# Kernel tuning notes

Measured on AMD Instinct MI355X. Metric: run time of the kernel, lower is better.

The kernel has to match this reference:

```python
import jax, jax.numpy as jnp
import numpy as np

ALPHA_LEAKY = 0.2
EPS = 1e-10


def setup_inputs() -> dict:
    key = jax.random.key(0)
    k1, k2, k3, k4 = jax.random.split(key, 4)
    N, E, IN_DIM, OUT_DIM = 50000, 800000, 128, 64
    node_features = jax.random.normal(k1, (N, IN_DIM), dtype=jnp.float32)
    edge_index = jax.random.randint(k2, (2, E), 0, N, dtype=jnp.int64)
    # xavier_uniform with gain=1.414
    def xavier(k, shape, gain=1.414):
        fan_in, fan_out = shape[1], shape[0]
        bound = gain * np.sqrt(6.0 / (fan_in + fan_out))
        return jax.random.uniform(k, shape, jnp.float32, -bound, bound)
    W = xavier(k3, (OUT_DIM, IN_DIM))          # nn.Linear weight layout [out, in]
    a = xavier(k4, (1, 2 * OUT_DIM))           # attention vector [1, 2*out]
    return {"node_features": node_features, "edge_index": edge_index, "W": W, "a": a}


def reference(node_features, edge_index, W, a):
    # h = W(node_features): [N, out_dim]
    h = node_features @ W.T
    num_nodes, out_dim = h.shape
    src = edge_index[0]
    tgt = edge_index[1]
    # a @ cat([h_src, h_tgt]) decomposes into per-node partial scores (no [E, 2d] concat)
    s_src = h @ a[0, :out_dim]   # [N]
    s_tgt = h @ a[0, out_dim:]   # [N]
    e = jax.nn.leaky_relu(s_src[src] + s_tgt[tgt], negative_slope=ALPHA_LEAKY)  # [E]
    # segment softmax over incoming edges of each target node
    e_max = jax.ops.segment_max(e, tgt, num_segments=num_nodes)
    e_exp = jnp.exp(e - e_max[tgt])
    e_sum = jax.ops.segment_sum(e_exp, tgt, num_segments=num_nodes)
    attention = e_exp / (e_sum[tgt] + EPS)
    # weighted scatter-add aggregation of source features into targets
    h_prime = jax.ops.segment_sum(h[src] * attention[:, None], tgt, num_segments=num_nodes)
    return jax.nn.elu(h_prime)
```

## Files before the change

### kernel.cpp

```cpp
#include <hip/hip_runtime.h>
#include <math.h>

#define ALPHA_LEAKY 0.2f
#define EPS_F 1e-10f
#define NBMAX 1024

typedef __attribute__((ext_vector_type(8))) short short8;
typedef __attribute__((ext_vector_type(4))) float f32x4;

__device__ __forceinline__ unsigned short bf16_rne(float f) {
    unsigned u = __float_as_uint(f);
    u += 0x7FFFu + ((u >> 16) & 1u);
    return (unsigned short)(u >> 16);
}

__global__ void k_prep(const float* __restrict__ W, uint4* __restrict__ Wbf) {
    int f = blockIdx.x * 256 + threadIdx.x;
    int nt = f >> 8;
    if (nt >= 4) return;
    int l = f & 63, kt = (f >> 6) & 3;
    int nn = nt * 16 + (l & 15);
    int k  = kt * 32 + (l >> 4) * 8;
    const float* wr = W + nn * 128 + k;
    unsigned short b[8];
    #pragma unroll
    for (int j = 0; j < 8; ++j) b[j] = bf16_rne(wr[j]);
    uint4 v;
    v.x = (unsigned)b[0] | ((unsigned)b[1] << 16);
    v.y = (unsigned)b[2] | ((unsigned)b[3] << 16);
    v.z = (unsigned)b[4] | ((unsigned)b[5] << 16);
    v.w = (unsigned)b[6] | ((unsigned)b[7] << 16);
    Wbf[f] = v;
}

__global__ __launch_bounds__(256) void k_gemm(
    const float* __restrict__ X, const uint4* __restrict__ Wbf,
    const float* __restrict__ a, unsigned short* __restrict__ hb,
    float* __restrict__ s_src, float* __restrict__ s_tgt, int n, int nstripes) {
    const int lane = threadIdx.x & 63;
    const int ml = lane & 15, g = lane >> 4;
    short8 bfr[4][4];
    #pragma unroll
    for (int nt = 0; nt < 4; ++nt)
        #pragma unroll
        for (int kt = 0; kt < 4; ++kt) {
            uint4 v = Wbf[(nt * 4 + kt) * 64 + lane];
            bfr[nt][kt] = *(short8*)&v;
        }
    float as[4], at[4];
    #pragma unroll
    for (int nt = 0; nt < 4; ++nt) {
        as[nt] = a[nt * 16 + ml];
        at[nt] = a[64 + nt * 16 + ml];
    }
    for (int stripe = blockIdx.x * 4 + (threadIdx.x >> 6); stripe < nstripes;
         stripe += gridDim.x * 4) {
        const int row0 = stripe * 16;
        const int rrow = min(row0 + ml, n - 1);
        const float* xr = X + (size_t)rrow * 128;
        f32x4 acc[4] = {{0.f,0.f,0.f,0.f},{0.f,0.f,0.f,0.f},
                        {0.f,0.f,0.f,0.f},{0.f,0.f,0.f,0.f}};
        #pragma unroll
        for (int kt = 0; kt < 4; ++kt) {
            float4 x0 = *(const float4*)(xr + kt * 32 + g * 8);
            float4 x1 = *(const float4*)(xr + kt * 32 + g * 8 + 4);
            short8 af;
            af[0] = (short)bf16_rne(x0.x); af[1] = (short)bf16_rne(x0.y);
            af[2] = (short)bf16_rne(x0.z); af[3] = (short)bf16_rne(x0.w);
            af[4] = (short)bf16_rne(x1.x); af[5] = (short)bf16_rne(x1.y);
            af[6] = (short)bf16_rne(x1.z); af[7] = (short)bf16_rne(x1.w);
            #pragma unroll
            for (int nt = 0; nt < 4; ++nt)
                acc[nt] = __builtin_amdgcn_mfma_f32_16x16x32_bf16(
                    af, bfr[nt][kt], acc[nt], 0, 0, 0);
        }
        #pragma unroll
        for (int reg = 0; reg < 4; ++reg) {
            int row = row0 + g * 4 + reg;
            float p = acc[0][reg] * as[0] + acc[1][reg] * as[1] +
                      acc[2][reg] * as[2] + acc[3][reg] * as[3];
            float q = acc[0][reg] * at[0] + acc[1][reg] * at[1] +
                      acc[2][reg] * at[2] + acc[3][reg] * at[3];
            #pragma unroll
            for (int off = 1; off < 16; off <<= 1) {
                p += __shfl_xor(p, off, 64);
                q += __shfl_xor(q, off, 64);
            }
            if (ml == 0 && row < n) { s_src[row] = p; s_tgt[row] = q; }
        }
        #pragma unroll
        for (int nt = 0; nt < 4; ++nt)
            #pragma unroll
            for (int reg = 0; reg < 4; ++reg) {
                int row = row0 + g * 4 + reg;
                if (row < n)
                    hb[(size_t)row * 64 + nt * 16 + ml] = bf16_rne(acc[nt][reg]);
            }
    }
}

__global__ __launch_bounds__(256) void k_hist(
    const int* __restrict__ ei, int* __restrict__ histg, int nb, int E, int epb) {
    __shared__ int hist[NBMAX];
    const int t = threadIdx.x;
    for (int k = t; k < nb; k += 256) hist[k] = 0;
    __syncthreads();
    const int e0 = blockIdx.x * epb, e1 = min(e0 + epb, E);
    for (int e = e0 + t; e < e1; e += 256)
        atomicAdd(&hist[ei[E + e] >> 6], 1);
    __syncthreads();
    int* outp = histg + (size_t)blockIdx.x * nb;
    for (int k = t; k < nb; k += 256) outp[k] = hist[k];
}

__global__ __launch_bounds__(256) void k_colscan(
    int* __restrict__ histg, int* __restrict__ btot, int nb) {
    __shared__ int wsum[4];
    const int bucket = blockIdx.x;
    const int t = threadIdx.x, lane = t & 63, w = t >> 6;
    int v = histg[(size_t)t * nb + bucket];
    int pre = v;
    #pragma unroll
    for (int off = 1; off < 64; off <<= 1) {
        int x = __shfl_up(pre, off, 64);
        if (lane >= off) pre += x;
    }
    if (lane == 63) wsum[w] = pre;
    __syncthreads();
    int wb = 0;
    for (int k = 0; k < w; ++k) wb += wsum[k];
    histg[(size_t)t * nb + bucket] = wb + pre - v;
    if (t == 255) btot[bucket] = wb + pre;
}

__global__ __launch_bounds__(256) void k_bscan(
    const int* __restrict__ btot, int* __restrict__ bstart, int nb, int E) {
    __shared__ int wsum[4];
    int t = threadIdx.x;
    int lane = t & 63, w = t >> 6;
    int v[4]; int sum = 0;
    #pragma unroll
    for (int j = 0; j < 4; ++j) {
        int idx = t * 4 + j;
        v[j] = (idx < nb) ? btot[idx] : 0;
        sum += v[j];
    }
    int pre = sum;
    #pragma unroll
    for (int off = 1; off < 64; off <<= 1) {
        int x = __shfl_up(pre, off, 64);
        if (lane >= off) pre += x;
    }
    if (lane == 63) wsum[w] = pre;
    __syncthreads();
    int wbase = 0;
    for (int k = 0; k < w; ++k) wbase += wsum[k];
    int run = wbase + pre - sum;
    #pragma unroll
    for (int j = 0; j < 4; ++j) {
        int idx = t * 4 + j;
        if (idx < nb) bstart[idx] = run;
        run += v[j];
    }
    if (t == 255) bstart[nb] = E;
}

__global__ __launch_bounds__(256) void k_place(
    const int* __restrict__ ei, const int* __restrict__ histg,
    const int* __restrict__ bstart, int2* __restrict__ st,
    int nb, int E, int epb) {
    __shared__ int cur[NBMAX];
    const int t = threadIdx.x;
    const int* my = histg + (size_t)blockIdx.x * nb;
    for (int k = t; k < nb; k += 256) cur[k] = bstart[k] + my[k];
    __syncthreads();
    const int e0 = blockIdx.x * epb, e1 = min(e0 + epb, E);
    for (int e = e0 + t; e < e1; e += 256) {
        int s  = ei[e];
        int tt = ei[E + e];
        int slot = atomicAdd(&cur[tt >> 6], 1);
        st[slot] = make_int2(s, tt);
    }
}

__global__ __launch_bounds__(256) void k_local(
    const int2* __restrict__ st, const int* __restrict__ bstart,
    int* __restrict__ base, int* __restrict__ deg, int* __restrict__ csr_src,
    int n) {
    __shared__ int hist[64];
    __shared__ int nbase[64];
    const int b = blockIdx.x;
    const int n0 = b << 6;
    const int t = threadIdx.x;
    if (t < 64) hist[t] = 0;
    __syncthreads();
    const int s0 = bstart[b], s1 = bstart[b + 1];
    for (int i = s0 + t; i < s1; i += 256)
        atomicAdd(&hist[st[i].y - n0], 1);
    __syncthreads();
    if (t < 64) {
        int v = hist[t];
        int pre = v;
        #pragma unroll
        for (int off = 1; off < 64; off <<= 1) {
            int x = __shfl_up(pre, off, 64);
            if (t >= off) pre += x;
        }
        int bs = s0 + pre - v;
        nbase[t] = bs;
        if (n0 + t < n) { base[n0 + t] = bs; deg[n0 + t] = v; }
    }
    __syncthreads();
    if (t < 64) hist[t] = nbase[t];
    __syncthreads();
    for (int i = s0 + t; i < s1; i += 256) {
        int2 e = st[i];
        int slot = atomicAdd(&hist[e.y - n0], 1);
        csr_src[slot] = e.x;
    }
}

__device__ __forceinline__ void accum8(float acc[8], uint4 hv, float w) {
    unsigned u[4] = {hv.x, hv.y, hv.z, hv.w};
    #pragma unroll
    for (int i = 0; i < 4; ++i) {
        float lo = __uint_as_float(u[i] << 16);
        float hi = __uint_as_float(u[i] & 0xFFFF0000u);
        acc[2 * i]     = fmaf(w, lo, acc[2 * i]);
        acc[2 * i + 1] = fmaf(w, hi, acc[2 * i + 1]);
    }
}

__global__ __launch_bounds__(256) void k_node(
    const int* __restrict__ base, const int* __restrict__ deg,
    const int* __restrict__ csr_src, const float* __restrict__ s_src,
    const float* __restrict__ s_tgt, const unsigned short* __restrict__ hb,
    float* __restrict__ out, int n) {
    const int lane = threadIdx.x & 63;
    const int node = blockIdx.x * 4 + (threadIdx.x >> 6);
    if (node >= n) return;
    const int b = base[node];
    const int d = deg[node];
    const float st = s_tgt[node];
    const int g = lane >> 3, r = lane & 7;
    float acc[8] = {0.f, 0.f, 0.f, 0.f, 0.f, 0.f, 0.f, 0.f};

    if (d <= 64) {
        int src_l = 0; float w_l = 0.f, v = -INFINITY;
        if (lane < d) {
            src_l = csr_src[b + lane];
            float x = s_src[src_l] + st;
            v = (x > 0.f) ? x : ALPHA_LEAKY * x;
        }
        float m = v;
        #pragma unroll
        for (int off = 32; off > 0; off >>= 1) m = fmaxf(m, __shfl_xor(m, off, 64));
        float ex = (lane < d) ? expf(v - m) : 0.f;
        float sum = ex;
        #pragma unroll
        for (int off = 32; off > 0; off >>= 1) sum += __shfl_xor(sum, off, 64);
        w_l = ex * (1.f / (sum + EPS_F));
        for (int k = 0; k < d; k += 8) {
            int ke = k + g;
            int s   = __shfl(src_l, ke, 64);
            float w = __shfl(w_l,  ke, 64);
            uint4 hv = ((const uint4*)(hb + (size_t)s * 64))[r];
            accum8(acc, hv, w);
        }
    } else {
        float m = -INFINITY;
        for (int c = lane; c < d; c += 64) {
            float x = s_src[csr_src[b + c]] + st;
            x = (x > 0.f) ? x : ALPHA_LEAKY * x;
            m = fmaxf(m, x);
        }
        #pragma unroll
        for (int off = 32; off > 0; off >>= 1) m = fmaxf(m, __shfl_xor(m, off, 64));
        float sum = 0.f;
        for (int c = lane; c < d; c += 64) {
            float x = s_src[csr_src[b + c]] + st;
            x = (x > 0.f) ? x : ALPHA_LEAKY * x;
            sum += expf(x - m);
        }
        #pragma unroll
        for (int off = 32; off > 0; off >>= 1) sum += __shfl_xor(sum, off, 64);
        float inv = 1.f / (sum + EPS_F);
        for (int c0 = 0; c0 < d; c0 += 64) {
            int j = c0 + lane;
            int src_l = 0; float w_l = 0.f;
            if (j < d) {
                src_l = csr_src[b + j];
                float x = s_src[src_l] + st;
                x = (x > 0.f) ? x : ALPHA_LEAKY * x;
                w_l = expf(x - m) * inv;
            }
            int lim = min(64, d - c0);
            for (int k = 0; k < lim; k += 8) {
                int ke = k + g;
                int s   = __shfl(src_l, ke, 64);
                float w = __shfl(w_l,  ke, 64);
                uint4 hv = ((const uint4*)(hb + (size_t)s * 64))[r];
                accum8(acc, hv, w);
            }
        }
    }

    #pragma unroll
    for (int off = 8; off <= 32; off <<= 1) {
        #pragma unroll
        for (int j = 0; j < 8; ++j) acc[j] += __shfl_xor(acc[j], off, 64);
    }
    if (g == 0) {
        float4 o0, o1;
        o0.x = acc[0] > 0.f ? acc[0] : expf(acc[0]) - 1.f;
        o0.y = acc[1] > 0.f ? acc[1] : expf(acc[1]) - 1.f;
        o0.z = acc[2] > 0.f ? acc[2] : expf(acc[2]) - 1.f;
        o0.w = acc[3] > 0.f ? acc[3] : expf(acc[3]) - 1.f;
        o1.x = acc[4] > 0.f ? acc[4] : expf(acc[4]) - 1.f;
        o1.y = acc[5] > 0.f ? acc[5] : expf(acc[5]) - 1.f;
        o1.z = acc[6] > 0.f ? acc[6] : expf(acc[6]) - 1.f;
        o1.w = acc[7] > 0.f ? acc[7] : expf(acc[7]) - 1.f;
        float4* o4 = (float4*)out + (size_t)node * 16;
        o4[r * 2]     = o0;
        o4[r * 2 + 1] = o1;
    }
}

extern "C" void kernel_launch(void* const* d_in, const int* in_sizes, int n_in,
                              void* d_out, int out_size, void* d_ws, size_t ws_size,
                              hipStream_t stream) {
    const float* X  = (const float*)d_in[0];
    const int*   ei = (const int*)d_in[1];
    const float* W  = (const float*)d_in[2];
    const float* a  = (const float*)d_in[3];
    float* out = (float*)d_out;

    const int N = in_sizes[0] / 128;
    const int E = in_sizes[1] / 2;
    const int nb = (N + 63) >> 6;
    const int NBLK = 256;
    const int epb = (E + NBLK - 1) / NBLK;

    char* p = (char*)d_ws;
    unsigned short* hb = (unsigned short*)p; p += (size_t)N * 64 * sizeof(unsigned short);
    uint4* Wbf    = (uint4*)p;  p += 1024 * sizeof(uint4);
    float* s_src  = (float*)p;  p += (size_t)N * sizeof(float);
    float* s_tgt  = (float*)p;  p += (size_t)N * sizeof(float);
    int*   deg    = (int*)p;    p += (size_t)N * sizeof(int);
    int*   base   = (int*)p;    p += (size_t)N * sizeof(int);
    int*   histg  = (int*)p;    p += (size_t)NBLK * nb * sizeof(int);
    int*   btot   = (int*)p;    p += (size_t)nb * sizeof(int);
    int*   bstart = (int*)p;    p += (size_t)(nb + 1) * sizeof(int);
    int*   csr_src= (int*)p;    p += (size_t)E * sizeof(int);
    int2*  st     = (int2*)p;

    const int nstripes = (N + 15) / 16;
    k_prep   <<<4, 256, 0, stream>>>(W, Wbf);
    k_gemm   <<<(nstripes + 3) / 4, 256, 0, stream>>>(X, Wbf, a, hb, s_src, s_tgt, N, nstripes);
    k_hist   <<<NBLK, 256, 0, stream>>>(ei, histg, nb, E, epb);
    k_colscan<<<nb, 256, 0, stream>>>(histg, btot, nb);
    k_bscan  <<<1, 256, 0, stream>>>(btot, bstart, nb, E);
    k_place  <<<NBLK, 256, 0, stream>>>(ei, histg, bstart, st, nb, E, epb);
    k_local  <<<nb, 256, 0, stream>>>(st, bstart, base, deg, csr_src, N);
    k_node   <<<(N + 3) / 4, 256, 0, stream>>>(base, deg, csr_src, s_src, s_tgt, hb, out, N);
}
```

Measured before the change: 146.7 us.

## Fuse local CSR build and node aggregation into bucket-level shared-memory kernel

```diff
diff --git a/kernel.cpp b/kernel.cpp
--- a/kernel.cpp
+++ b/kernel.cpp
@@ -4,6 +4,7 @@
 #define ALPHA_LEAKY 0.2f
 #define EPS_F 1e-10f
 #define NBMAX 1024
+#define NBLK 128
 
 typedef __attribute__((ext_vector_type(8))) short short8;
 typedef __attribute__((ext_vector_type(4))) float f32x4;
@@ -118,7 +119,7 @@
     __shared__ int wsum[4];
     const int bucket = blockIdx.x;
     const int t = threadIdx.x, lane = t & 63, w = t >> 6;
-    int v = histg[(size_t)t * nb + bucket];
+    int v = (t < NBLK) ? histg[(size_t)t * nb + bucket] : 0;
     int pre = v;
     #pragma unroll
     for (int off = 1; off < 64; off <<= 1) {
@@ -129,8 +130,8 @@
     __syncthreads();
     int wb = 0;
     for (int k = 0; k < w; ++k) wb += wsum[k];
-    histg[(size_t)t * nb + bucket] = wb + pre - v;
-    if (t == 255) btot[bucket] = wb + pre;
+    if (t < NBLK) histg[(size_t)t * nb + bucket] = wb + pre - v;
+    if (t == 255) btot[bucket] = wsum[0] + wsum[1] + wsum[2] + wsum[3];
 }
 
 __global__ __launch_bounds__(256) void k_bscan(
@@ -167,7 +168,7 @@
 
 __global__ __launch_bounds__(256) void k_place(
     const int* __restrict__ ei, const int* __restrict__ histg,
-    const int* __restrict__ bstart, int2* __restrict__ st,
+    const int* __restrict__ bstart, unsigned* __restrict__ st,
     int nb, int E, int epb) {
     __shared__ int cur[NBMAX];
     const int t = threadIdx.x;
@@ -179,150 +180,67 @@
         int s  = ei[e];
         int tt = ei[E + e];
         int slot = atomicAdd(&cur[tt >> 6], 1);
-        st[slot] = make_int2(s, tt);
-    }
-}
-
-__global__ __launch_bounds__(256) void k_local(
-    const int2* __restrict__ st, const int* __restrict__ bstart,
-    int* __restrict__ base, int* __restrict__ deg, int* __restrict__ csr_src,
-    int n) {
-    __shared__ int hist[64];
-    __shared__ int nbase[64];
+        st[slot] = ((unsigned)s << 6) | (unsigned)(tt & 63);
+    }
+}
+
+__global__ __launch_bounds__(256) void k_bnode(
+    const unsigned* __restrict__ st, const int* __restrict__ bstart,
+    const float* __restrict__ s_src, const float* __restrict__ s_tgt,
+    const unsigned short* __restrict__ hb, float* __restrict__ out, int n) {
+    __shared__ unsigned mkey[64];
+    __shared__ float msh[64];
+    __shared__ float ssum[64];
+    __shared__ float acc[64 * 64];
     const int b = blockIdx.x;
     const int n0 = b << 6;
     const int t = threadIdx.x;
-    if (t < 64) hist[t] = 0;
-    __syncthreads();
+    const int lane = t & 63;
+    const int w = t >> 6;
+
+    if (t < 64) { mkey[t] = 0u; ssum[t] = 0.f; }
+    for (int i = t; i < 4096; i += 256) acc[i] = 0.f;
+    __syncthreads();
+
     const int s0 = bstart[b], s1 = bstart[b + 1];
-    for (int i = s0 + t; i < s1; i += 256)
-        atomicAdd(&hist[st[i].y - n0], 1);
+
+    for (int i = s0 + t; i < s1; i += 256) {
+        unsigned p = st[i];
+        int s = p >> 6, dt = p & 63;
+        float x = s_src[s] + s_tgt[n0 + dt];
+        x = (x > 0.f) ? x : ALPHA_LEAKY * x;
+        unsigned u = __float_as_uint(x);
+        unsigned key = (u & 0x80000000u) ? ~u : (u | 0x80000000u);
+        atomicMax(&mkey[dt], key);
+    }
     __syncthreads();
     if (t < 64) {
-        int v = hist[t];
-        int pre = v;
-        #pragma unroll
-        for (int off = 1; off < 64; off <<= 1) {
-            int x = __shfl_up(pre, off, 64);
-            if (t >= off) pre += x;
-        }
-        int bs = s0 + pre - v;
-        nbase[t] = bs;
-        if (n0 + t < n) { base[n0 + t] = bs; deg[n0 + t] = v; }
-    }
-    __syncthreads();
-    if (t < 64) hist[t] = nbase[t];
-    __syncthreads();
-    for (int i = s0 + t; i < s1; i += 256) {
-        int2 e = st[i];
-        int slot = atomicAdd(&hist[e.y - n0], 1);
-        csr_src[slot] = e.x;
-    }
-}
-
-__device__ __forceinline__ void accum8(float acc[8], uint4 hv, float w) {
-    unsigned u[4] = {hv.x, hv.y, hv.z, hv.w};
-    #pragma unroll
-    for (int i = 0; i < 4; ++i) {
-        float lo = __uint_as_float(u[i] << 16);
-        float hi = __uint_as_float(u[i] & 0xFFFF0000u);
-        acc[2 * i]     = fmaf(w, lo, acc[2 * i]);
-        acc[2 * i + 1] = fmaf(w, hi, acc[2 * i + 1]);
-    }
-}
-
-__global__ __launch_bounds__(256) void k_node(
-    const int* __restrict__ base, const int* __restrict__ deg,
-    const int* __restrict__ csr_src, const float* __restrict__ s_src,
-    const float* __restrict__ s_tgt, const unsigned short* __restrict__ hb,
-    float* __restrict__ out, int n) {
-    const int lane = threadIdx.x & 63;
-    const int node = blockIdx.x * 4 + (threadIdx.x >> 6);
-    if (node >= n) return;
-    const int b = base[node];
-    const int d = deg[node];
-    const float st = s_tgt[node];
-    const int g = lane >> 3, r = lane & 7;
-    float acc[8] = {0.f, 0.f, 0.f, 0.f, 0.f, 0.f, 0.f, 0.f};
-
-    if (d <= 64) {
-        int src_l = 0; float w_l = 0.f, v = -INFINITY;
-        if (lane < d) {
-            src_l = csr_src[b + lane];
-            float x = s_src[src_l] + st;
-            v = (x > 0.f) ? x : ALPHA_LEAKY * x;
-        }
-        float m = v;
-        #pragma unroll
-        for (int off = 32; off > 0; off >>= 1) m = fmaxf(m, __shfl_xor(m, off, 64));
-        float ex = (lane < d) ? expf(v - m) : 0.f;
-        float sum = ex;
-        #pragma unroll
-        for (int off = 32; off > 0; off >>= 1) sum += __shfl_xor(sum, off, 64);
-        w_l = ex * (1.f / (sum + EPS_F));
-        for (int k = 0; k < d; k += 8) {
-            int ke = k + g;
-            int s   = __shfl(src_l, ke, 64);
-            float w = __shfl(w_l,  ke, 64);
-            uint4 hv = ((const uint4*)(hb + (size_t)s * 64))[r];
-            accum8(acc, hv, w);
-        }
-    } else {
-        float m = -INFINITY;
-        for (int c = lane; c < d; c += 64) {
-            float x = s_src[csr_src[b + c]] + st;
-            x = (x > 0.f) ? x : ALPHA_LEAKY * x;
-            m = fmaxf(m, x);
-        }
-        #pragma unroll
-        for (int off = 32; off > 0; off >>= 1) m = fmaxf(m, __shfl_xor(m, off, 64));
-        float sum = 0.f;
-        for (int c = lane; c < d; c += 64) {
-            float x = s_src[csr_src[b + c]] + st;
-            x = (x > 0.f) ? x : ALPHA_LEAKY * x;
-            sum += expf(x - m);
-        }
-        #pragma unroll
-        for (int off = 32; off > 0; off >>= 1) sum += __shfl_xor(sum, off, 64);
-        float inv = 1.f / (sum + EPS_F);
-        for (int c0 = 0; c0 < d; c0 += 64) {
-            int j = c0 + lane;
-            int src_l = 0; float w_l = 0.f;
-            if (j < d) {
-                src_l = csr_src[b + j];
-                float x = s_src[src_l] + st;
-                x = (x > 0.f) ? x : ALPHA_LEAKY * x;
-                w_l = expf(x - m) * inv;
-            }
-            int lim = min(64, d - c0);
-            for (int k = 0; k < lim; k += 8) {
-                int ke = k + g;
-                int s   = __shfl(src_l, ke, 64);
-                float w = __shfl(w_l,  ke, 64);
-                uint4 hv = ((const uint4*)(hb + (size_t)s * 64))[r];
-                accum8(acc, hv, w);
-            }
-        }
-    }
-
-    #pragma unroll
-    for (int off = 8; off <= 32; off <<= 1) {
-        #pragma unroll
-        for (int j = 0; j < 8; ++j) acc[j] += __shfl_xor(acc[j], off, 64);
-    }
-    if (g == 0) {
-        float4 o0, o1;
-        o0.x = acc[0] > 0.f ? acc[0] : expf(acc[0]) - 1.f;
-        o0.y = acc[1] > 0.f ? acc[1] : expf(acc[1]) - 1.f;
-        o0.z = acc[2] > 0.f ? acc[2] : expf(acc[2]) - 1.f;
-        o0.w = acc[3] > 0.f ? acc[3] : expf(acc[3]) - 1.f;
-        o1.x = acc[4] > 0.f ? acc[4] : expf(acc[4]) - 1.f;
-        o1.y = acc[5] > 0.f ? acc[5] : expf(acc[5]) - 1.f;
-        o1.z = acc[6] > 0.f ? acc[6] : expf(acc[6]) - 1.f;
-        o1.w = acc[7] > 0.f ? acc[7] : expf(acc[7]) - 1.f;
-        float4* o4 = (float4*)out + (size_t)node * 16;
-        o4[r * 2]     = o0;
-        o4[r * 2 + 1] = o1;
+        unsigned key = mkey[t];
+        unsigned u = (key & 0x80000000u) ? (key & 0x7FFFFFFFu) : ~key;
+        msh[t] = __uint_as_float(u);
+    }
+    __syncthreads();
+
+    for (int i = s0 + w; i < s1; i += 4) {
+        unsigned p = st[i];
+        int s = p >> 6, dt = p & 63;
+        float x = s_src[s] + s_tgt[n0 + dt];
+        x = (x > 0.f) ? x : ALPHA_LEAKY * x;
+        float we = expf(x - msh[dt]);
+        if (lane == 0) atomicAdd(&ssum[dt], we);
+        unsigned short hraw = hb[(size_t)s * 64 + lane];
+        float hv = __uint_as_float((unsigned)hraw << 16);
+        atomicAdd(&acc[dt * 64 + lane], we * hv);
+    }
+    __syncthreads();
+
+    for (int i = t; i < 4096; i += 256) {
+        int node = i >> 6;
+        int nn = n0 + node;
+        if (nn < n) {
+            float v = acc[i] / (ssum[node] + EPS_F);
+            out[(size_t)n0 * 64 + i] = (v > 0.f) ? v : expf(v) - 1.f;
+        }
     }
 }
 
@@ -338,21 +256,17 @@
     const int N = in_sizes[0] / 128;
     const int E = in_sizes[1] / 2;
     const int nb = (N + 63) >> 6;
-    const int NBLK = 256;
     const int epb = (E + NBLK - 1) / NBLK;
 
     char* p = (char*)d_ws;
     unsigned short* hb = (unsigned short*)p; p += (size_t)N * 64 * sizeof(unsigned short);
-    uint4* Wbf    = (uint4*)p;  p += 1024 * sizeof(uint4);
-    float* s_src  = (float*)p;  p += (size_t)N * sizeof(float);
-    float* s_tgt  = (float*)p;  p += (size_t)N * sizeof(float);
-    int*   deg    = (int*)p;    p += (size_t)N * sizeof(int);
-    int*   base   = (int*)p;    p += (size_t)N * sizeof(int);
-    int*   histg  = (int*)p;    p += (size_t)NBLK * nb * sizeof(int);
-    int*   btot   = (int*)p;    p += (size_t)nb * sizeof(int);
-    int*   bstart = (int*)p;    p += (size_t)(nb + 1) * sizeof(int);
-    int*   csr_src= (int*)p;    p += (size_t)E * sizeof(int);
-    int2*  st     = (int2*)p;
+    uint4*    Wbf    = (uint4*)p;    p += 1024 * sizeof(uint4);
+    float*    s_src  = (float*)p;    p += (size_t)N * sizeof(float);
+    float*    s_tgt  = (float*)p;    p += (size_t)N * sizeof(float);
+    int*      histg  = (int*)p;      p += (size_t)NBLK * nb * sizeof(int);
+    int*      btot   = (int*)p;      p += (size_t)nb * sizeof(int);
+    int*      bstart = (int*)p;      p += (size_t)(nb + 1) * sizeof(int);
+    unsigned* st     = (unsigned*)p;
 
     const int nstripes = (N + 15) / 16;
     k_prep   <<<4, 256, 0, stream>>>(W, Wbf);
@@ -361,6 +275,5 @@
     k_colscan<<<nb, 256, 0, stream>>>(histg, btot, nb);
     k_bscan  <<<1, 256, 0, stream>>>(btot, bstart, nb, E);
     k_place  <<<NBLK, 256, 0, stream>>>(ei, histg, bstart, st, nb, E, epb);
-    k_local  <<<nb, 256, 0, stream>>>(st, bstart, base, deg, csr_src, N);
-    k_node   <<<(N + 3) / 4, 256, 0, stream>>>(base, deg, csr_src, s_src, s_tgt, hb, out, N);
-}
+    k_bnode  <<<nb, 256, 0, stream>>>(st, bstart, s_src, s_tgt, hb, out, N);
+}
```

Result: slower. 504.2 us (+243.7%).
